# Kernel optimization log

Measured on AMD Instinct MI355X. Metric: run time of the kernel, lower is better.

## Reference

```python
import jax, jax.numpy as jnp
import numpy as np


def _conv3d(x, w):
    # x: [N, C, D, H, W], w: [O, I, K, K, K] -> [N, O, D', H', W'] VALID conv
    return jax.lax.conv_general_dilated(
        x, w, window_strides=(1, 1, 1), padding='VALID',
        dimension_numbers=('NCDHW', 'OIDHW', 'NCDHW'))


def conv4d(x, w):
    # x: [B, C, D1, D2, D3, D4]; w: [O, I, K1, K2, K3, K4]
    # Decompose 4D conv as a sum over K1 taps of 3D convs; the sliced D1
    # window is folded into the batch dimension so XLA's 3D conv does the work.
    B, C, D1, D2, D3, D4 = x.shape
    O, I, K1, K2, K3, K4 = w.shape
    D1o = D1 - K1 + 1
    out = None
    for i in range(K1):  # small fixed loop over kernel taps (K1=3)
        xs = jax.lax.dynamic_slice_in_dim(x, i, D1o, axis=2)      # [B,C,D1o,D2,D3,D4]
        xs = xs.transpose(0, 2, 1, 3, 4, 5).reshape(B * D1o, C, D2, D3, D4)
        y = _conv3d(xs, w[:, :, i])                                # [B*D1o,O,d2,d3,d4]
        out = y if out is None else out + y
    d2, d3, d4 = out.shape[2], out.shape[3], out.shape[4]
    out = out.reshape(B, D1o, O, d2, d3, d4).transpose(0, 2, 1, 3, 4, 5)
    return out  # [B, O, D1o, d2, d3, d4]


def setup_inputs() -> dict:
    key = jax.random.key(0)
    k1, k2 = jax.random.split(key)
    pic_in = jax.random.normal(k1, (2, 16, 8, 8, 64, 64), dtype=jnp.float32)
    # convNd weight: [out_channels, in_channels, K, K, K, K], no bias
    weight = jax.random.normal(k2, (32, 16, 3, 3, 3, 3), dtype=jnp.float32) * 0.05
    return {"pic_in": pic_in, "weight": weight}


def reference(pic_in, weight):
    # ConvKernel.forward: 4D conv (stride 1, padding 0, no bias) + ReLU
    return jax.nn.relu(conv4d(pic_in, weight))
```

## Files before the change

### kernel.cpp

```cpp
#include <hip/hip_runtime.h>


typedef __attribute__((ext_vector_type(8))) __bf16 bf16x8;
typedef __attribute__((ext_vector_type(16))) float f32x16;

#define CSTRIDE 262144

#define WT_OFF 0
#define XB_OFF 131072

__global__ __launch_bounds__(256) void prep(const float* __restrict__ x,
                                            const float* __restrict__ w,
                                            unsigned char* __restrict__ ws) {
  int blk = blockIdx.x;
  if (blk < 512) {
    __bf16* xb = (__bf16*)(ws + XB_OFF);
    int n = blk * 256 + threadIdx.x;
    int cg = n & 15;
    int d3 = (n >> 4) & 63;
    int d2 = (n >> 10) & 7;
    int d1 = (n >> 13) & 7;
    int b = n >> 16;
    const float* gx =
        x + ((((b * 16) * 8 + d1) * 8 + d2) * 64 + d3) * 64 + cg * 4;
    float4 v[16];
#pragma unroll
    for (int c = 0; c < 16; ++c)
      v[c] = *(const float4*)(gx + (size_t)c * CSTRIDE);
    __bf16* row = xb + ((((b * 8 + d1) * 8 + d2) * 64 + d3) * 1024);
#pragma unroll
    for (int ch = 0; ch < 2; ++ch) {
#pragma unroll
      for (int j = 0; j < 4; ++j) {
        bf16x8 o;
#pragma unroll
        for (int cc = 0; cc < 8; ++cc)
          o[cc] = (__bf16)(((const float*)&v[ch * 8 + cc])[j]);
        *(bf16x8*)(row + ch * 512 + (cg * 4 + j) * 8) = o;
      }
    }
  } else {
    int o = blk - 512;
    __bf16* wT = (__bf16*)(ws + WT_OFF);
#pragma unroll
    for (int base = 0; base < 1296; base += 256) {
      int idx = base + threadIdx.x;
      if (idx < 1296) {
        int c = idx / 81, t = idx % 81;
        wT[t * 512 + o * 16 + c] = (__bf16)w[o * 1296 + idx];
      }
    }
  }
}

__global__ __launch_bounds__(256, 4) void conv_mfma(
    const unsigned char* __restrict__ ws, float* __restrict__ out) {
  const unsigned char* wTb = ws + WT_OFF;
  const unsigned char* xbb = ws + XB_OFF;

  int bid = blockIdx.x;
  int g = bid % 72;
  int chunk = bid / 72;
  int b = g / 36;
  int e1 = (g / 6) % 6;
  int e2 = g % 6;
  int r0 = chunk * 4;

  int lane = threadIdx.x & 63;
  int wave = threadIdx.x >> 6;
  int th = wave & 1;
  int kp = wave >> 1;
  int m32 = lane & 31;
  int half = lane >> 5;

  int aoff = half * 1024 + (th * 32 + m32) * 16;
  int woff = m32 * 32 + half * 16;

  f32x16 acc[4];
#pragma unroll
  for (int i = 0; i < 4; ++i)
#pragma unroll
    for (int r = 0; r < 16; ++r) acc[i][r] = 0.f;

  int p0 = kp ? 4 : 0;
  int p1 = kp ? 9 : 4;
  for (int p = p0; p < p1; ++p) {
    int k1 = (p >= 3) + (p >= 6);
    int k2 = p - k1 * 3;
    const unsigned char* abase =
        xbb + (size_t)(((b * 8 + e1 + k1) * 8 + e2 + k2) * 64 + r0) * 2048 +
        aoff;
    const unsigned char* wbase = wTb + p * 9216 + woff;
#pragma unroll
    for (int k4 = 0; k4 < 3; ++k4) {
      bf16x8 arow[6];
#pragma unroll
      for (int j = 0; j < 6; ++j)
        arow[j] = *(const bf16x8*)(abase + j * 2048 + k4 * 16);
#pragma unroll
      for (int k3 = 0; k3 < 3; ++k3) {
        bf16x8 bf = *(const bf16x8*)(wbase + (k3 * 3 + k4) * 1024);
#pragma unroll
        for (int i = 0; i < 4; ++i)
          acc[i] = __builtin_amdgcn_mfma_f32_32x32x16_bf16(arow[i + k3], bf,
                                                           acc[i], 0, 0, 0);
      }
    }
  }

  __shared__ float sc[2][32 * 33];
  float* s = sc[th];
  int e4 = th * 32 + m32;
  size_t obase =
      ((((size_t)b * 32) * 6 + e1) * 6 + e2) * 3844;
#pragma unroll
  for (int i = 0; i < 4; ++i) {
    __syncthreads();
    if (kp == 1) {
#pragma unroll
      for (int r = 0; r < 16; ++r) {
        int m = (r & 3) + 8 * (r >> 2) + 4 * half;
        s[m * 33 + m32] = acc[i][r];
      }
    }
    __syncthreads();
    if (kp == 0) {
#pragma unroll
      for (int r = 0; r < 16; ++r) {
        int m = (r & 3) + 8 * (r >> 2) + 4 * half;
        s[m * 33 + m32] += acc[i][r];
      }
      int e3 = r0 + i;
      if (e3 < 62) {
#pragma unroll
        for (int it = 0; it < 16; ++it) {
          int o = it * 2 + half;
          float v = fmaxf(s[m32 * 33 + o], 0.f);
          if (e4 < 62)
            out[obase + (size_t)o * 138384 + (size_t)e3 * 62 + e4] = v;
        }
      }
    }
  }
}

extern "C" void kernel_launch(void* const* d_in, const int* in_sizes, int n_in,
                              void* d_out, int out_size, void* d_ws,
                              size_t ws_size, hipStream_t stream) {
  const float* x = (const float*)d_in[0];
  const float* w = (const float*)d_in[1];
  float* out = (float*)d_out;
  unsigned char* ws = (unsigned char*)d_ws;
  prep<<<dim3(544), dim3(256), 0, stream>>>(x, w, ws);
  conv_mfma<<<dim3(16 * 72), dim3(256), 0, stream>>>(ws, out);
}
```

Baseline: 132.9 us.

## Split waves over output rows and double-buffer A/B register loads

```diff
diff --git a/kernel.cpp b/kernel.cpp
--- a/kernel.cpp
+++ b/kernel.cpp
@@ -53,7 +53,7 @@
   }
 }
 
-__global__ __launch_bounds__(256, 4) void conv_mfma(
+__global__ __launch_bounds__(256, 2) void conv_mfma(
     const unsigned char* __restrict__ ws, float* __restrict__ out) {
   const unsigned char* wTb = ws + WT_OFF;
   const unsigned char* xbb = ws + XB_OFF;
@@ -64,17 +64,21 @@
   int b = g / 36;
   int e1 = (g / 6) % 6;
   int e2 = g % 6;
-  int r0 = chunk * 4;
+  int r0 = chunk * 8;
 
   int lane = threadIdx.x & 63;
   int wave = threadIdx.x >> 6;
   int th = wave & 1;
-  int kp = wave >> 1;
+  int rg = wave >> 1;
   int m32 = lane & 31;
   int half = lane >> 5;
 
   int aoff = half * 1024 + (th * 32 + m32) * 16;
   int woff = m32 * 32 + half * 16;
+
+  const unsigned char* abase0 =
+      xbb + (size_t)(((b * 8 + e1) * 8 + e2) * 64 + r0 + rg * 4) * 2048 + aoff;
+  const unsigned char* wbase = wTb + woff;
 
   f32x16 acc[4];
 #pragma unroll
@@ -82,63 +86,68 @@
 #pragma unroll
     for (int r = 0; r < 16; ++r) acc[i][r] = 0.f;
 
-  int p0 = kp ? 4 : 0;
-  int p1 = kp ? 9 : 4;
-  for (int p = p0; p < p1; ++p) {
-    int k1 = (p >= 3) + (p >= 6);
-    int k2 = p - k1 * 3;
-    const unsigned char* abase =
-        xbb + (size_t)(((b * 8 + e1 + k1) * 8 + e2 + k2) * 64 + r0) * 2048 +
-        aoff;
-    const unsigned char* wbase = wTb + p * 9216 + woff;
+  bf16x8 ab[2][6];
+  bf16x8 bb[2][9];
+
+#pragma unroll
+  for (int j = 0; j < 6; ++j)
+    ab[0][j] = *(const bf16x8*)(abase0 + j * 2048);
+#pragma unroll
+  for (int t9 = 0; t9 < 9; ++t9)
+    bb[0][t9] = *(const bf16x8*)(wbase + t9 * 1024);
+
+#pragma unroll
+  for (int p = 0; p < 9; ++p) {
+    const int k1 = p / 3, k2 = p % 3;
+    const unsigned char* acur = abase0 + (k1 * 8 + k2) * 131072;
 #pragma unroll
     for (int k4 = 0; k4 < 3; ++k4) {
-      bf16x8 arow[6];
+      const int sc = (p * 3 + k4) & 1, sn = sc ^ 1;
+      if (k4 < 2) {
 #pragma unroll
-      for (int j = 0; j < 6; ++j)
-        arow[j] = *(const bf16x8*)(abase + j * 2048 + k4 * 16);
+        for (int j = 0; j < 6; ++j)
+          ab[sn][j] = *(const bf16x8*)(acur + j * 2048 + (k4 + 1) * 16);
+      } else if (p < 8) {
+        const int nk1 = (p + 1) / 3, nk2 = (p + 1) % 3;
+        const unsigned char* anxt = abase0 + (nk1 * 8 + nk2) * 131072;
+#pragma unroll
+        for (int j = 0; j < 6; ++j)
+          ab[sn][j] = *(const bf16x8*)(anxt + j * 2048);
+#pragma unroll
+        for (int t9 = 0; t9 < 9; ++t9)
+          bb[(p + 1) & 1][t9] =
+              *(const bf16x8*)(wbase + (p + 1) * 9216 + t9 * 1024);
+      }
 #pragma unroll
       for (int k3 = 0; k3 < 3; ++k3) {
-        bf16x8 bf = *(const bf16x8*)(wbase + (k3 * 3 + k4) * 1024);
+        bf16x8 bf = bb[p & 1][k3 * 3 + k4];
 #pragma unroll
         for (int i = 0; i < 4; ++i)
-          acc[i] = __builtin_amdgcn_mfma_f32_32x32x16_bf16(arow[i + k3], bf,
+          acc[i] = __builtin_amdgcn_mfma_f32_32x32x16_bf16(ab[sc][i + k3], bf,
                                                            acc[i], 0, 0, 0);
       }
     }
   }
 
-  __shared__ float sc[2][32 * 33];
-  float* s = sc[th];
+  __shared__ float scr[4][32 * 33];
+  float* s = scr[wave];
   int e4 = th * 32 + m32;
-  size_t obase =
-      ((((size_t)b * 32) * 6 + e1) * 6 + e2) * 3844;
+  size_t obase = ((((size_t)b * 32) * 6 + e1) * 6 + e2) * 3844;
 #pragma unroll
   for (int i = 0; i < 4; ++i) {
-    __syncthreads();
-    if (kp == 1) {
+    int e3 = r0 + rg * 4 + i;
 #pragma unroll
-      for (int r = 0; r < 16; ++r) {
-        int m = (r & 3) + 8 * (r >> 2) + 4 * half;
-        s[m * 33 + m32] = acc[i][r];
-      }
+    for (int r = 0; r < 16; ++r) {
+      int m = (r & 3) + 8 * (r >> 2) + 4 * half;
+      s[m * 33 + m32] = acc[i][r];
     }
-    __syncthreads();
-    if (kp == 0) {
+    if (e3 < 62) {
 #pragma unroll
-      for (int r = 0; r < 16; ++r) {
-        int m = (r & 3) + 8 * (r >> 2) + 4 * half;
-        s[m * 33 + m32] += acc[i][r];
-      }
-      int e3 = r0 + i;
-      if (e3 < 62) {
-#pragma unroll
-        for (int it = 0; it < 16; ++it) {
-          int o = it * 2 + half;
-          float v = fmaxf(s[m32 * 33 + o], 0.f);
-          if (e4 < 62)
-            out[obase + (size_t)o * 138384 + (size_t)e3 * 62 + e4] = v;
-        }
+      for (int it = 0; it < 16; ++it) {
+        int o = it * 2 + half;
+        float v = fmaxf(s[m32 * 33 + o], 0.f);
+        if (e4 < 62)
+          out[obase + (size_t)o * 138384 + (size_t)e3 * 62 + e4] = v;
       }
     }
   }
@@ -152,5 +161,5 @@
   float* out = (float*)d_out;
   unsigned char* ws = (unsigned char*)d_ws;
   prep<<<dim3(544), dim3(256), 0, stream>>>(x, w, ws);
-  conv_mfma<<<dim3(16 * 72), dim3(256), 0, stream>>>(ws, out);
+  conv_mfma<<<dim3(8 * 72), dim3(256), 0, stream>>>(ws, out);
 }
```

New measurement: 130.3 us. No clear change (-1.9%).
